# Kernel optimization log

Hardware: AMD Instinct MI355X
Metric: run time of the kernel (lower is better)

Reference implementation:

```python
import jax, jax.numpy as jnp
import numpy as np

N_NODES = 50000
N_EDGES = 800000
F_DIM = 64
AVG_D_LOG = 2.833  # avg_d['log'] ~ log(avg_degree + 1)
EPS_STD = 1e-5     # PNA std aggregator epsilon
EPS_BN = 1e-5      # BatchNorm1d epsilon


def setup_inputs() -> dict:
    key = jax.random.key(0)
    k = jax.random.split(key, 5)
    h = jax.random.normal(k[0], (N_NODES, F_DIM), dtype=jnp.float32)
    src = jax.random.randint(k[1], (N_EDGES,), 0, N_NODES)
    dst = jax.random.randint(k[2], (N_EDGES,), 0, N_NODES)
    # posttrans: single Linear(12*F, F) (posttrans_layers=1, last_activation='none')
    W = jax.random.normal(k[3], (12 * F_DIM, F_DIM), dtype=jnp.float32) * 0.02
    b = jnp.zeros((F_DIM,), dtype=jnp.float32)
    gamma = jnp.ones((F_DIM,), dtype=jnp.float32)
    beta = jnp.zeros((F_DIM,), dtype=jnp.float32)
    return {"h": h, "src": src, "dst": dst, "W": W, "b": b, "gamma": gamma, "beta": beta}


def reference(h, src, dst, W, b, gamma, beta):
    N = h.shape[0]
    m = h[src]  # [E, F] messages: copy_u
    ones = jnp.ones((src.shape[0],), dtype=h.dtype)
    deg = jax.ops.segment_sum(ones, dst, num_segments=N)            # [N]
    s = jax.ops.segment_sum(m, dst, num_segments=N)                 # [N, F]
    s2 = jax.ops.segment_sum(m * m, dst, num_segments=N)            # [N, F]
    mx = jax.ops.segment_max(m, dst, num_segments=N)                # [N, F]
    mn = jax.ops.segment_min(m, dst, num_segments=N)                # [N, F]

    degc = jnp.maximum(deg, 1.0)[:, None]
    mean = s / degc
    var = jax.nn.relu(s2 / degc - mean * mean)
    std = jnp.sqrt(var + EPS_STD)

    # aggregator concat (dim=1): [mean | max | min | std] -> [N, 4F]
    agg = jnp.concatenate([mean, mx, mn, std], axis=1)
    has = (deg > 0)[:, None]
    agg = jnp.where(has, agg, 0.0)  # DGL zero-fills zero-in-degree nodes

    logD = jnp.log(deg + 1.0)[:, None]
    amp = agg * (logD / AVG_D_LOG)
    att = agg * jnp.where(has, AVG_D_LOG / jnp.maximum(logD, 1e-12), 0.0)

    # scaler concat: [identity | amplification | attenuation] -> [N, 12F]
    x = jnp.concatenate([agg, amp, att], axis=1)

    # posttrans linear
    x = x @ W + b

    # BatchNorm1d (training-mode batch statistics)
    mu = jnp.mean(x, axis=0)
    v = jnp.var(x, axis=0)
    x = gamma * (x - mu) / jnp.sqrt(v + EPS_BN) + beta

    x = jax.nn.relu(x)
    x = h + x  # residual (in_dim == out_dim)
    # dropout p=0.0 -> identity
    return x
```

## Files before the change

### kernel.cpp

```cpp
#include <hip/hip_runtime.h>
#include <hip/hip_bf16.h>

#define NND 50000
#define NED 800000
#define FD 64
#define PADW 64
#define MPAD2 50176
#define NBLK 196
#define NEBLK 3125
#define NXCD 8
#define NPX 6250
#define AVGDL 2.833f

typedef __attribute__((ext_vector_type(8))) short short8;
typedef __attribute__((ext_vector_type(4))) short short4v;
typedef __attribute__((ext_vector_type(4))) float floatx4;

__global__ __launch_bounds__(256) void prep(const float* __restrict__ W,
                                            __hip_bfloat16* __restrict__ Wf,
                                            int* __restrict__ deg,
                                            float* __restrict__ gsum,
                                            float* __restrict__ gsumsq,
                                            __hip_bfloat16* __restrict__ aggb) {
    int i = blockIdx.x * 256 + threadIdx.x;
    if (i < NND) deg[i] = 0;
    if (i < 64) { gsum[i] = 0.f; gsumsq[i] = 0.f; }
    if (i < (MPAD2 - NND) * 128) ((unsigned int*)(aggb + (size_t)NND * 256))[i] = 0u;
    if (i < 8 * 12 * 64 * 8) {
        int e = i & 7;
        int l = (i >> 3) & 63;
        int st = i >> 9;
        int t = st % 12, s5 = st / 12;
        int k = 32 * s5 + (l >> 4) * 8 + e;
        int col = 16 * t + (l & 15);
        int g = col >> 6, jj = col & 63;
        Wf[i] = __float2bfloat16(W[(g * 256 + k) * FD + jj]);
    }
}

__global__ __launch_bounds__(256) void fill_csr(const int* __restrict__ src,
                                                const int* __restrict__ dst,
                                                int* __restrict__ deg,
                                                int* __restrict__ csr) {
    int g = blockIdx.x & (NXCD - 1);
    int e = (blockIdx.x >> 3) * 256 + threadIdx.x;
    if (e < NED) {
        int d = dst[e];
        if ((unsigned)(d - g * NPX) < (unsigned)NPX) {
            int slot = atomicAdd(&deg[d], 1);
            if (slot < PADW) csr[d * PADW + slot] = src[e];
        }
    }
}

__global__ __launch_bounds__(256) void aggregate(
    const float* __restrict__ h, const int* __restrict__ deg,
    const int* __restrict__ csr, __hip_bfloat16* __restrict__ aggb,
    float* __restrict__ c1, float* __restrict__ c2) {
    int wid = blockIdx.x * 4 + (threadIdx.x >> 6);
    int lane = threadIdx.x & 63;
    if (wid >= NND) return;
    int d = deg[wid];
    if (d > PADW) d = PADW;
    int q = lane & 15, sub = lane >> 4;
    const float* hq = h + 4 * q;
    floatx4 s  = (floatx4){0.f, 0.f, 0.f, 0.f};
    floatx4 s2 = (floatx4){0.f, 0.f, 0.f, 0.f};
    floatx4 mx = (floatx4){-INFINITY, -INFINITY, -INFINITY, -INFINITY};
    floatx4 mn = (floatx4){INFINITY, INFINITY, INFINITY, INFINITY};
    float cc1 = 0.f, cc2 = 0.f;
    floatx4 statv = (floatx4){0.f, 0.f, 0.f, 0.f};
    if (d > 0) {
        const int* row_idx = csr + wid * PADW;
        int myidx = row_idx[lane < d ? lane : d - 1];
        for (int j = 0; j < d; j += 8) {
            int jc0 = j + sub;     jc0 = jc0 < d ? jc0 : d - 1;
            int jc1 = j + 4 + sub; jc1 = jc1 < d ? jc1 : d - 1;
            int i0 = __shfl(myidx, jc0);
            int i1 = __shfl(myidx, jc1);
            floatx4 v0 = *(const floatx4*)(&hq[(size_t)i0 * FD]);
            floatx4 v1 = *(const floatx4*)(&hq[(size_t)i1 * FD]);
            #pragma unroll
            for (int k = 0; k < 4; ++k) {
                s[k] += v0[k] + v1[k];
                s2[k] += v0[k] * v0[k];
                s2[k] += v1[k] * v1[k];
                mx[k] = fmaxf(mx[k], fmaxf(v0[k], v1[k]));
                mn[k] = fminf(mn[k], fminf(v0[k], v1[k]));
            }
        }
        #pragma unroll
        for (int m = 16; m <= 32; m <<= 1) {
            #pragma unroll
            for (int k = 0; k < 4; ++k) {
                s[k]  += __shfl_xor(s[k], m);
                s2[k] += __shfl_xor(s2[k], m);
                mx[k] = fmaxf(mx[k], __shfl_xor(mx[k], m));
                mn[k] = fminf(mn[k], __shfl_xor(mn[k], m));
            }
        }
        int npad = (8 - (d & 7)) & 7;
        if (npad > 0) {
            int il = __shfl(myidx, d - 1);
            floatx4 vl = *(const floatx4*)(&hq[(size_t)il * FD]);
            float np = (float)npad;
            #pragma unroll
            for (int k = 0; k < 4; ++k) {
                s[k]  -= np * vl[k];
                s2[k] -= np * vl[k] * vl[k];
            }
        }
        float degf = (float)d;
        float inv = 1.f / degf;
        #pragma unroll
        for (int k = 0; k < 4; ++k) {
            float mean = s[k] * inv;
            float var = fmaxf(s2[k] * inv - mean * mean, 0.f);
            float stdv = sqrtf(var + 1e-5f);
            statv[k] = (sub == 0) ? mean : (sub == 1) ? mx[k] : (sub == 2) ? mn[k] : stdv;
        }
        float logD = logf(degf + 1.f);
        cc1 = logD / AVGDL;
        cc2 = AVGDL / fmaxf(logD, 1e-12f);
    }
    union { __hip_bfloat16 b[4]; short4v v; } u;
    #pragma unroll
    for (int k = 0; k < 4; ++k) u.b[k] = __float2bfloat16(statv[k]);
    *(short4v*)(aggb + (size_t)wid * 256 + sub * 64 + 4 * q) = u.v;
    if (lane == 0) { c1[wid] = cc1; c2[wid] = cc2; }
}

__global__ __launch_bounds__(512) void gemm_kernel(
    const __hip_bfloat16* __restrict__ aggb, const __hip_bfloat16* __restrict__ Wf,
    const float* __restrict__ c1, const float* __restrict__ c2,
    const float* __restrict__ bias,
    float* __restrict__ x, float* __restrict__ gsum, float* __restrict__ gsumsq) {
    __shared__ short8 Bsm[6144];
    __shared__ float cs[64], css[64];
    int tid = threadIdx.x;
    const short8* Wf8 = (const short8*)Wf;
    #pragma unroll
    for (int i = 0; i < 12; ++i) Bsm[i * 512 + tid] = Wf8[i * 512 + tid];
    if (tid < 64) { cs[tid] = 0.f; css[tid] = 0.f; }
    __syncthreads();

    int w = tid >> 6, lane = tid & 63;
    int c = lane & 15, hi = lane >> 4;
    int rowBase = blockIdx.x * 256 + w * 32;
    const short8* A8 = (const short8*)aggb;

    floatx4 acc[2][12];
    #pragma unroll
    for (int p = 0; p < 2; ++p)
        #pragma unroll
        for (int t = 0; t < 12; ++t) acc[p][t] = (floatx4){0.f, 0.f, 0.f, 0.f};

    #pragma unroll
    for (int s5 = 0; s5 < 8; ++s5) {
        short8 a0 = A8[(size_t)(rowBase + c) * 32 + 4 * s5 + hi];
        short8 a1 = A8[(size_t)(rowBase + 16 + c) * 32 + 4 * s5 + hi];
        #pragma unroll
        for (int t = 0; t < 12; ++t) {
            short8 b = Bsm[(s5 * 12 + t) * 64 + lane];
            acc[0][t] = __builtin_amdgcn_mfma_f32_16x16x32_bf16(a0, b, acc[0][t], 0, 0, 0);
            acc[1][t] = __builtin_amdgcn_mfma_f32_16x16x32_bf16(a1, b, acc[1][t], 0, 0, 0);
        }
    }

    float bv[4];
    #pragma unroll
    for (int t = 0; t < 4; ++t) bv[t] = bias[16 * t + c];
    float psum[4] = {0.f, 0.f, 0.f, 0.f}, psq[4] = {0.f, 0.f, 0.f, 0.f};
    #pragma unroll
    for (int p = 0; p < 2; ++p) {
        #pragma unroll
        for (int r = 0; r < 4; ++r) {
            int row = rowBase + p * 16 + hi * 4 + r;
            bool valid = row < NND;
            float c1v = valid ? c1[row] : 0.f;
            float c2v = valid ? c2[row] : 0.f;
            #pragma unroll
            for (int t = 0; t < 4; ++t) {
                float val = acc[p][t][r] + c1v * acc[p][t + 4][r] + c2v * acc[p][t + 8][r] + bv[t];
                if (valid) {
                    x[(size_t)row * FD + 16 * t + c] = val;
                    psum[t] += val;
                    psq[t] += val * val;
                }
            }
        }
    }
    #pragma unroll
    for (int t = 0; t < 4; ++t) {
        float rs = psum[t], rq = psq[t];
        rs += __shfl_xor(rs, 16); rs += __shfl_xor(rs, 32);
        rq += __shfl_xor(rq, 16); rq += __shfl_xor(rq, 32);
        if (hi == 0) { atomicAdd(&cs[16 * t + c], rs); atomicAdd(&css[16 * t + c], rq); }
    }
    __syncthreads();
    if (tid < 64) { atomicAdd(&gsum[tid], cs[tid]); atomicAdd(&gsumsq[tid], css[tid]); }
}

__global__ __launch_bounds__(256) void finalize(
    const float* __restrict__ x, const float* __restrict__ h,
    const float* __restrict__ gsum, const float* __restrict__ gsumsq,
    const float* __restrict__ gamma, const float* __restrict__ beta,
    float* __restrict__ out) {
    __shared__ float sc[64], sh[64];
    int tid = threadIdx.x;
    if (tid < 64) {
        float mu = gsum[tid] * (1.f / NND);
        float var = gsumsq[tid] * (1.f / NND) - mu * mu;
        float s = gamma[tid] * rsqrtf(var + 1e-5f);
        sc[tid] = s;
        sh[tid] = beta[tid] - mu * s;
    }
    __syncthreads();
    int i = blockIdx.x * 256 + tid;
    if (i >= NND * FD / 4) return;
    int jj = (i & 15) * 4;
    floatx4 xv = ((const floatx4*)x)[i];
    floatx4 hv = ((const floatx4*)h)[i];
    floatx4 o;
    #pragma unroll
    for (int q = 0; q < 4; ++q) {
        float v = sc[jj + q] * xv[q] + sh[jj + q];
        o[q] = hv[q] + fmaxf(v, 0.f);
    }
    ((floatx4*)out)[i] = o;
}

extern "C" void kernel_launch(void* const* d_in, const int* in_sizes, int n_in,
                              void* d_out, int out_size, void* d_ws, size_t ws_size,
                              hipStream_t stream) {
    const float* h     = (const float*)d_in[0];
    const int*   src   = (const int*)d_in[1];
    const int*   dst   = (const int*)d_in[2];
    const float* W     = (const float*)d_in[3];
    const float* bias  = (const float*)d_in[4];
    const float* gamma = (const float*)d_in[5];
    const float* beta  = (const float*)d_in[6];
    float* out = (float*)d_out;

    char* ws = (char*)d_ws;
    size_t off = 0;
    auto alloc = [&](size_t bytes) -> char* {
        char* p = ws + off;
        off = (off + bytes + 255) & ~(size_t)255;
        return p;
    };
    int* deg        = (int*)alloc(NND * 4);
    int* csr        = (int*)alloc((size_t)NND * PADW * 4);
    float* c1       = (float*)alloc(MPAD2 * 4);
    float* c2       = (float*)alloc(MPAD2 * 4);
    __hip_bfloat16* aggb = (__hip_bfloat16*)alloc((size_t)MPAD2 * 256 * 2);
    __hip_bfloat16* Wf   = (__hip_bfloat16*)alloc(8 * 12 * 64 * 8 * 2);
    float* x        = (float*)alloc((size_t)NND * FD * 4);
    float* gsum     = (float*)alloc(64 * 4);
    float* gsumsq   = (float*)alloc(64 * 4);

    prep<<<NBLK, 256, 0, stream>>>(W, Wf, deg, gsum, gsumsq, aggb);
    fill_csr<<<NEBLK * NXCD, 256, 0, stream>>>(src, dst, deg, csr);
    aggregate<<<(NND + 3) / 4, 256, 0, stream>>>(h, deg, csr, aggb, c1, c2);
    gemm_kernel<<<NBLK, 512, 0, stream>>>(aggb, Wf, c1, c2, bias, x, gsum, gsumsq);
    finalize<<<(NND * FD / 4 + 255) / 256, 256, 0, stream>>>(x, h, gsum, gsumsq, gamma, beta, out);
}
```

Baseline: 173.1 us.

## Gather bf16 copy of node features and vectorize CSR edge loads

Adds a pass that converts h to bf16 so the aggregation gather moves half as many bytes per neighbor row, and the sum, sum of squares, max and min are still accumulated in fp32. fill_csr now has each thread load four src/dst entries as int4 vectors, which cuts block count and per-edge load instructions. The extra conversion kernel costs a read of h and a write of the bf16 copy. Aggregate statistics, and std in particular, lose precision because inputs are rounded to bf16.

```diff
diff --git a/kernel.cpp b/kernel.cpp
--- a/kernel.cpp
+++ b/kernel.cpp
@@ -7,7 +7,7 @@
 #define PADW 64
 #define MPAD2 50176
 #define NBLK 196
-#define NEBLK 3125
+#define NE4BLK 782
 #define NXCD 8
 #define NPX 6250
 #define AVGDL 2.833f
@@ -15,6 +15,11 @@
 typedef __attribute__((ext_vector_type(8))) short short8;
 typedef __attribute__((ext_vector_type(4))) short short4v;
 typedef __attribute__((ext_vector_type(4))) float floatx4;
+typedef __attribute__((ext_vector_type(4))) int int4v;
+
+__device__ __forceinline__ float b2f(short u) {
+    return __uint_as_float(((unsigned)(unsigned short)u) << 16);
+}
 
 __global__ __launch_bounds__(256) void prep(const float* __restrict__ W,
                                             __hip_bfloat16* __restrict__ Wf,
@@ -38,23 +43,51 @@
     }
 }
 
+__global__ __launch_bounds__(256) void hconv(const float* __restrict__ h,
+                                             __hip_bfloat16* __restrict__ hb) {
+    int i = blockIdx.x * 256 + threadIdx.x;
+    if (i >= NND * FD / 8) return;
+    floatx4 a = ((const floatx4*)h)[2 * i];
+    floatx4 b = ((const floatx4*)h)[2 * i + 1];
+    union { __hip_bfloat16 x[8]; short8 v; } u;
+    #pragma unroll
+    for (int k = 0; k < 4; ++k) {
+        u.x[k] = __float2bfloat16(a[k]);
+        u.x[4 + k] = __float2bfloat16(b[k]);
+    }
+    ((short8*)hb)[i] = u.v;
+}
+
 __global__ __launch_bounds__(256) void fill_csr(const int* __restrict__ src,
                                                 const int* __restrict__ dst,
                                                 int* __restrict__ deg,
                                                 int* __restrict__ csr) {
     int g = blockIdx.x & (NXCD - 1);
-    int e = (blockIdx.x >> 3) * 256 + threadIdx.x;
-    if (e < NED) {
-        int d = dst[e];
-        if ((unsigned)(d - g * NPX) < (unsigned)NPX) {
-            int slot = atomicAdd(&deg[d], 1);
-            if (slot < PADW) csr[d * PADW + slot] = src[e];
+    int e = (blockIdx.x >> 3) * 1024 + threadIdx.x * 4;
+    if (e + 3 < NED) {
+        int4v d4 = *(const int4v*)(&dst[e]);
+        int4v s4 = *(const int4v*)(&src[e]);
+        #pragma unroll
+        for (int k = 0; k < 4; ++k) {
+            int d = d4[k];
+            if ((unsigned)(d - g * NPX) < (unsigned)NPX) {
+                int slot = atomicAdd(&deg[d], 1);
+                if (slot < PADW) csr[d * PADW + slot] = s4[k];
+            }
+        }
+    } else if (e < NED) {
+        for (int k = 0; k < 4 && e + k < NED; ++k) {
+            int d = dst[e + k];
+            if ((unsigned)(d - g * NPX) < (unsigned)NPX) {
+                int slot = atomicAdd(&deg[d], 1);
+                if (slot < PADW) csr[d * PADW + slot] = src[e + k];
+            }
         }
     }
 }
 
 __global__ __launch_bounds__(256) void aggregate(
-    const float* __restrict__ h, const int* __restrict__ deg,
+    const __hip_bfloat16* __restrict__ hb, const int* __restrict__ deg,
     const int* __restrict__ csr, __hip_bfloat16* __restrict__ aggb,
     float* __restrict__ c1, float* __restrict__ c2) {
     int wid = blockIdx.x * 4 + (threadIdx.x >> 6);
@@ -63,7 +96,7 @@
     int d = deg[wid];
     if (d > PADW) d = PADW;
     int q = lane & 15, sub = lane >> 4;
-    const float* hq = h + 4 * q;
+    const __hip_bfloat16* hq = hb + 4 * q;
     floatx4 s  = (floatx4){0.f, 0.f, 0.f, 0.f};
     floatx4 s2 = (floatx4){0.f, 0.f, 0.f, 0.f};
     floatx4 mx = (floatx4){-INFINITY, -INFINITY, -INFINITY, -INFINITY};
@@ -78,15 +111,17 @@
             int jc1 = j + 4 + sub; jc1 = jc1 < d ? jc1 : d - 1;
             int i0 = __shfl(myidx, jc0);
             int i1 = __shfl(myidx, jc1);
-            floatx4 v0 = *(const floatx4*)(&hq[(size_t)i0 * FD]);
-            floatx4 v1 = *(const floatx4*)(&hq[(size_t)i1 * FD]);
+            short4v r0 = *(const short4v*)(&hq[(size_t)i0 * FD]);
+            short4v r1 = *(const short4v*)(&hq[(size_t)i1 * FD]);
             #pragma unroll
             for (int k = 0; k < 4; ++k) {
-                s[k] += v0[k] + v1[k];
-                s2[k] += v0[k] * v0[k];
-                s2[k] += v1[k] * v1[k];
-                mx[k] = fmaxf(mx[k], fmaxf(v0[k], v1[k]));
-                mn[k] = fminf(mn[k], fminf(v0[k], v1[k]));
+                float a = b2f(r0[k]);
+                float b = b2f(r1[k]);
+                s[k] += a + b;
+                s2[k] += a * a;
+                s2[k] += b * b;
+                mx[k] = fmaxf(mx[k], fmaxf(a, b));
+                mn[k] = fminf(mn[k], fminf(a, b));
             }
         }
         #pragma unroll
@@ -102,12 +137,13 @@
         int npad = (8 - (d & 7)) & 7;
         if (npad > 0) {
             int il = __shfl(myidx, d - 1);
-            floatx4 vl = *(const floatx4*)(&hq[(size_t)il * FD]);
+            short4v rl = *(const short4v*)(&hq[(size_t)il * FD]);
             float np = (float)npad;
             #pragma unroll
             for (int k = 0; k < 4; ++k) {
-                s[k]  -= np * vl[k];
-                s2[k] -= np * vl[k] * vl[k];
+                float vl = b2f(rl[k]);
+                s[k]  -= np * vl;
+                s2[k] -= np * vl * vl;
             }
         }
         float degf = (float)d;
@@ -251,6 +287,7 @@
     };
     int* deg        = (int*)alloc(NND * 4);
     int* csr        = (int*)alloc((size_t)NND * PADW * 4);
+    __hip_bfloat16* hb = (__hip_bfloat16*)alloc((size_t)NND * FD * 2);
     float* c1       = (float*)alloc(MPAD2 * 4);
     float* c2       = (float*)alloc(MPAD2 * 4);
     __hip_bfloat16* aggb = (__hip_bfloat16*)alloc((size_t)MPAD2 * 256 * 2);
@@ -260,8 +297,9 @@
     float* gsumsq   = (float*)alloc(64 * 4);
 
     prep<<<NBLK, 256, 0, stream>>>(W, Wf, deg, gsum, gsumsq, aggb);
-    fill_csr<<<NEBLK * NXCD, 256, 0, stream>>>(src, dst, deg, csr);
-    aggregate<<<(NND + 3) / 4, 256, 0, stream>>>(h, deg, csr, aggb, c1, c2);
+    hconv<<<(NND * FD / 8 + 255) / 256, 256, 0, stream>>>(h, hb);
+    fill_csr<<<NE4BLK * NXCD, 256, 0, stream>>>(src, dst, deg, csr);
+    aggregate<<<(NND + 3) / 4, 256, 0, stream>>>(hb, deg, csr, aggb, c1, c2);
     gemm_kernel<<<NBLK, 512, 0, stream>>>(aggb, Wf, c1, c2, bias, x, gsum, gsumsq);
     finalize<<<(NND * FD / 4 + 255) / 256, 256, 0, stream>>>(x, h, gsum, gsumsq, gamma, beta, out);
 }
```

Measured after the change: 178.5 us. 3.1% more time.
